# Kernel tuning notes

Measured on AMD Instinct MI355X. Metric: run time of the kernel, lower is better.

## Reference

```python
import jax, jax.numpy as jnp
import numpy as np

DIM = 1024
HEADS = 16
DIM_HEAD = 64
INNER = HEADS * DIM_HEAD
SCALE = DIM_HEAD ** -0.5


def rotate_half(t):
    # '... (j d) -> ... j d' with j=2: split last dim in half
    x1, x2 = jnp.split(t, 2, axis=-1)
    return jnp.concatenate((-x2, x1), axis=-1)


def rotary_pos(n, d, dtype):
    inv_freq = 1.0 / (10000.0 ** (jnp.arange(0, d, 2, dtype=jnp.float32) / d))
    freqs = jnp.arange(n, dtype=jnp.float32)[:, None] * inv_freq[None, :]  # (n, d/2)
    return jnp.concatenate((freqs, freqs), axis=-1).astype(dtype)  # (n, d)


def apply_rope(pos, t):
    return t * jnp.cos(pos) + rotate_half(t) * jnp.sin(pos)


def setup_inputs() -> dict:
    key = jax.random.key(0)
    ks = jax.random.split(key, 5)
    x = jax.random.normal(ks[0], (2, 2048, DIM), dtype=jnp.float32)
    gamma = jnp.ones((DIM,), dtype=jnp.float32)
    beta = jnp.zeros((DIM,), dtype=jnp.float32)
    Wq = jax.random.normal(ks[1], (DIM, INNER), dtype=jnp.float32) * 0.02
    Wkv = jax.random.normal(ks[2], (DIM, 2 * INNER), dtype=jnp.float32) * 0.02
    Wo = jax.random.normal(ks[3], (INNER, DIM), dtype=jnp.float32) * 0.02
    return {"x": x, "gamma": gamma, "beta": beta, "Wq": Wq, "Wkv": Wkv, "Wo": Wo}


def reference(x, gamma, beta, Wq, Wkv, Wo):
    b, n, _ = x.shape
    # LayerNorm with learned gamma, fixed-zero beta buffer
    mu = jnp.mean(x, axis=-1, keepdims=True)
    var = jnp.var(x, axis=-1, keepdims=True)
    xn = (x - mu) / jnp.sqrt(var + 1e-5) * gamma + beta

    q = xn @ Wq                       # (b, n, inner)
    kv = xn @ Wkv
    k, v = jnp.split(kv, 2, axis=-1)

    def to_heads(t):
        return t.reshape(b, n, HEADS, DIM_HEAD).transpose(0, 2, 1, 3)  # b h n d

    q, k, v = map(to_heads, (q, k, v))

    pos = rotary_pos(n, DIM_HEAD, x.dtype)  # (n, d)
    q = apply_rope(pos, q)
    k = apply_rope(pos, k)

    q = q * SCALE
    sim = jnp.einsum('bhid,bhjd->bhij', q, k)

    neg = -jnp.finfo(sim.dtype).max
    causal_mask = jnp.triu(jnp.ones((n, n), dtype=bool), k=1)
    sim = jnp.where(causal_mask, neg, sim)

    attn = jax.nn.softmax(sim, axis=-1)
    out = jnp.einsum('bhij,bhjd->bhid', attn, v)
    out = out.transpose(0, 2, 1, 3).reshape(b, n, INNER)
    return out @ Wo
```

## Files before the change

kernel.cpp:

```cpp
#include <hip/hip_runtime.h>
#include <stdint.h>

typedef unsigned short u16;
typedef __attribute__((ext_vector_type(8))) short short8;
typedef __attribute__((ext_vector_type(4))) float floatx4;
typedef __attribute__((ext_vector_type(4))) unsigned short u16x4;
typedef __attribute__((ext_vector_type(2))) unsigned int uint2v;

__device__ __forceinline__ float bf2f(u16 v) {
  union { uint32_t u; float f; } x; x.u = ((uint32_t)v) << 16; return x.f;
}
__device__ __forceinline__ u16 f2bf(float f) {
  union { float f; uint32_t u; } x; x.f = f;
  uint32_t r = x.u + 0x7fffu + ((x.u >> 16) & 1u);
  return (u16)(r >> 16);
}
__device__ __forceinline__ uint32_t fu(float f) {
  union { float f; uint32_t u; } x; x.f = f; return x.u;
}

#define GL2LDS(g, l)                                                          \
  __builtin_amdgcn_global_load_lds(                                           \
      (const __attribute__((address_space(1))) void*)(g),                     \
      (__attribute__((address_space(3))) void*)(l), 16, 0, 0)

__global__ __launch_bounds__(256) void transpose_w3_k(const float* __restrict__ Wq,
                                                      const float* __restrict__ Wkv,
                                                      const float* __restrict__ Wo,
                                                      u16* __restrict__ wqkvT,
                                                      u16* __restrict__ woT) {
  __shared__ float tile[32][33];
  int z = blockIdx.z;
  const float* in = (z == 0) ? Wq : (z == 1) ? Wkv : Wo;
  u16* out = (z == 0) ? wqkvT : (z == 1) ? (wqkvT + 1024 * 1024) : woT;
  int C = (z == 1) ? 2048 : 1024;
  int c0 = blockIdx.x * 32, r0 = blockIdx.y * 32;
  if (c0 >= C) return;
  int tx = threadIdx.x, ty = threadIdx.y;
#pragma unroll
  for (int i = 0; i < 32; i += 8)
    tile[ty + i][tx] = in[(size_t)(r0 + ty + i) * C + c0 + tx];
  __syncthreads();
#pragma unroll
  for (int i = 0; i < 32; i += 8)
    out[(size_t)(c0 + ty + i) * 1024 + r0 + tx] = f2bf(tile[tx][ty + i]);
}

__global__ __launch_bounds__(256) void layernorm_k(const float* __restrict__ x,
                                                   const float* __restrict__ gamma,
                                                   const float* __restrict__ beta,
                                                   u16* __restrict__ xn) {
  int row = blockIdx.x;
  int t = threadIdx.x;
  const float* xr = x + (size_t)row * 1024;
  float4 xv = *(const float4*)(xr + t * 4);
  float v0 = xv.x, v1 = xv.y, v2 = xv.z, v3 = xv.w;
  float s = v0 + v1 + v2 + v3;
  float s2 = v0 * v0 + v1 * v1 + v2 * v2 + v3 * v3;
#pragma unroll
  for (int d = 1; d < 64; d <<= 1) {
    s += __shfl_xor(s, d, 64);
    s2 += __shfl_xor(s2, d, 64);
  }
  __shared__ float red[8];
  int lane = t & 63, wv = t >> 6;
  if (lane == 0) { red[wv] = s; red[4 + wv] = s2; }
  __syncthreads();
  s = red[0] + red[1] + red[2] + red[3];
  s2 = red[4] + red[5] + red[6] + red[7];
  float mu = s * (1.0f / 1024.0f);
  float var = s2 * (1.0f / 1024.0f) - mu * mu;
  float rstd = rsqrtf(var + 1e-5f);
  float4 gv = *(const float4*)(gamma + t * 4);
  float4 bv = *(const float4*)(beta + t * 4);
  u16x4 ov;
  ov.x = f2bf((v0 - mu) * rstd * gv.x + bv.x);
  ov.y = f2bf((v1 - mu) * rstd * gv.y + bv.y);
  ov.z = f2bf((v2 - mu) * rstd * gv.z + bv.z);
  ov.w = f2bf((v3 - mu) * rstd * gv.w + bv.w);
  *(u16x4*)(xn + (size_t)row * 1024 + t * 4) = ov;
}

__global__ __launch_bounds__(256) void gemm_bf16_k(const u16* __restrict__ A,
                                                   const u16* __restrict__ BT,
                                                   void* __restrict__ Cp,
                                                   int K, int lda, int ldc,
                                                   int f32out) {
  __shared__ __align__(16) u16 lA[128 * 32];
  __shared__ __align__(16) u16 lB[128 * 32];
  int tid = threadIdx.x;
  int bm = blockIdx.y * 128;
  int bn = blockIdx.x * 128;
  int w = tid >> 6, l = tid & 63;
  int wm = (w >> 1) * 64, wn = (w & 1) * 64;
  int lr = l & 15, lq = l >> 4;
  floatx4 acc[4][4] = {};
  int sr = w * 16 + (l >> 2);
  int sc = (l & 3) * 8;
  for (int k0 = 0; k0 < K; k0 += 32) {
    GL2LDS(A + (size_t)(bm + sr) * lda + k0 + sc, &lA[sr * 32 + sc]);
    GL2LDS(A + (size_t)(bm + sr + 64) * lda + k0 + sc, &lA[(sr + 64) * 32 + sc]);
    GL2LDS(BT + (size_t)(bn + sr) * K + k0 + sc, &lB[sr * 32 + sc]);
    GL2LDS(BT + (size_t)(bn + sr + 64) * K + k0 + sc, &lB[(sr + 64) * 32 + sc]);
    __syncthreads();
    short8 afr[4], bfr[4];
#pragma unroll
    for (int i = 0; i < 4; i++)
      afr[i] = *(const short8*)(&lA[(wm + i * 16 + lr) * 32 + lq * 8]);
#pragma unroll
    for (int i = 0; i < 4; i++)
      bfr[i] = *(const short8*)(&lB[(wn + i * 16 + lr) * 32 + lq * 8]);
#pragma unroll
    for (int mi = 0; mi < 4; mi++)
#pragma unroll
      for (int ni = 0; ni < 4; ni++)
        acc[mi][ni] = __builtin_amdgcn_mfma_f32_16x16x32_bf16(
            afr[mi], bfr[ni], acc[mi][ni], 0, 0, 0);
    __syncthreads();
  }
  if (f32out) {
    float* Cf = (float*)Cp;
#pragma unroll
    for (int mi = 0; mi < 4; mi++)
#pragma unroll
      for (int ni = 0; ni < 4; ni++)
#pragma unroll
        for (int r = 0; r < 4; r++) {
          int row = bm + wm + mi * 16 + lq * 4 + r;
          int col = bn + wn + ni * 16 + lr;
          Cf[(size_t)row * ldc + col] = acc[mi][ni][r];
        }
  } else {
    u16* Cb = (u16*)Cp;
#pragma unroll
    for (int mi = 0; mi < 4; mi++)
#pragma unroll
      for (int ni = 0; ni < 4; ni++)
#pragma unroll
        for (int r = 0; r < 4; r++) {
          int row = bm + wm + mi * 16 + lq * 4 + r;
          int col = bn + wn + ni * 16 + lr;
          Cb[(size_t)row * ldc + col] = f2bf(acc[mi][ni][r]);
        }
  }
}

__global__ __launch_bounds__(256) void gemm64_bf16_k(const u16* __restrict__ A,
                                                     const u16* __restrict__ BT,
                                                     float* __restrict__ C,
                                                     int K, int lda, int ldc) {
  __shared__ __align__(16) u16 lA[64 * 32];
  __shared__ __align__(16) u16 lB[128 * 32];
  int tid = threadIdx.x;
  int bm = blockIdx.y * 64;
  int bn = blockIdx.x * 128;
  int w = tid >> 6, l = tid & 63;
  int wm = (w >> 1) * 32, wn = (w & 1) * 64;
  int lr = l & 15, lq = l >> 4;
  floatx4 acc[2][4] = {};
  int sr = w * 16 + (l >> 2);
  int sc = (l & 3) * 8;
  for (int k0 = 0; k0 < K; k0 += 32) {
    GL2LDS(A + (size_t)(bm + sr) * lda + k0 + sc, &lA[sr * 32 + sc]);
    GL2LDS(BT + (size_t)(bn + sr) * K + k0 + sc, &lB[sr * 32 + sc]);
    GL2LDS(BT + (size_t)(bn + sr + 64) * K + k0 + sc, &lB[(sr + 64) * 32 + sc]);
    __syncthreads();
    short8 afr[2], bfr[4];
#pragma unroll
    for (int i = 0; i < 2; i++)
      afr[i] = *(const short8*)(&lA[(wm + i * 16 + lr) * 32 + lq * 8]);
#pragma unroll
    for (int i = 0; i < 4; i++)
      bfr[i] = *(const short8*)(&lB[(wn + i * 16 + lr) * 32 + lq * 8]);
#pragma unroll
    for (int mi = 0; mi < 2; mi++)
#pragma unroll
      for (int ni = 0; ni < 4; ni++)
        acc[mi][ni] = __builtin_amdgcn_mfma_f32_16x16x32_bf16(
            afr[mi], bfr[ni], acc[mi][ni], 0, 0, 0);
    __syncthreads();
  }
#pragma unroll
  for (int mi = 0; mi < 2; mi++)
#pragma unroll
    for (int ni = 0; ni < 4; ni++)
#pragma unroll
      for (int r = 0; r < 4; r++) {
        int row = bm + wm + mi * 16 + lq * 4 + r;
        int col = bn + wn + ni * 16 + lr;
        C[(size_t)row * ldc + col] = acc[mi][ni][r];
      }
}

__global__ __launch_bounds__(256) void rope_vt_k(u16* __restrict__ qkv,
                                                 u16* __restrict__ vT) {
  int bid = blockIdx.x;
  if (bid < 2048) {
    int idx = bid * 256 + threadIdx.x;
    int ig = idx & 7;
    int h = (idx >> 3) & 15;
    int row = idx >> 7;
    int n = row & 2047;
    int i0 = ig * 4;
    const float QS = 0.125f * 1.44269504088896f;
    float c_[4], s_[4];
    float invf = exp2f(-(float)i0 * 0.4152410118609203f);
    const float rstep = 0.74989420933245582f;
#pragma unroll
    for (int e = 0; e < 4; e++) {
      float ang = (float)n * invf;
      c_[e] = cosf(ang);
      s_[e] = sinf(ang);
      invf *= rstep;
    }
    size_t base = (size_t)row * 3072 + h * 64 + i0;
    u16x4 qlo = *(u16x4*)(qkv + base);
    u16x4 qhi = *(u16x4*)(qkv + base + 32);
    u16x4 klo = *(u16x4*)(qkv + base + 1024);
    u16x4 khi = *(u16x4*)(qkv + base + 1056);
    u16x4 oqlo, oqhi, oklo, okhi;
#pragma unroll
    for (int e = 0; e < 4; e++) {
      float x1 = bf2f(((u16*)&qlo)[e]), x2 = bf2f(((u16*)&qhi)[e]);
      ((u16*)&oqlo)[e] = f2bf((x1 * c_[e] - x2 * s_[e]) * QS);
      ((u16*)&oqhi)[e] = f2bf((x2 * c_[e] + x1 * s_[e]) * QS);
      x1 = bf2f(((u16*)&klo)[e]); x2 = bf2f(((u16*)&khi)[e]);
      ((u16*)&oklo)[e] = f2bf(x1 * c_[e] - x2 * s_[e]);
      ((u16*)&okhi)[e] = f2bf(x2 * c_[e] + x1 * s_[e]);
    }
    *(u16x4*)(qkv + base) = oqlo;
    *(u16x4*)(qkv + base + 32) = oqhi;
    *(u16x4*)(qkv + base + 1024) = oklo;
    *(u16x4*)(qkv + base + 1056) = okhi;
  } else {
    __shared__ u16 tile[32][33];
    int vb = bid - 2048;
    int bh = vb >> 7;
    int rest = vb & 127;
    int d0 = (rest >> 6) * 32;
    int n0 = (rest & 63) * 32;
    int b = bh >> 4, h = bh & 15;
    int tid = threadIdx.x;
    int tx = tid & 31, ty = tid >> 5;
#pragma unroll
    for (int i = 0; i < 32; i += 8)
      tile[ty + i][tx] =
          qkv[(size_t)(b * 2048 + n0 + ty + i) * 3072 + 2048 + h * 64 + d0 + tx];
    __syncthreads();
#pragma unroll
    for (int i = 0; i < 32; i += 8)
      vT[((size_t)bh * 64 + d0 + ty + i) * 2048 + n0 + tx] = tile[tx][ty + i];
  }
}

#define LPT 72
__device__ __forceinline__ void attn_tile2(const short8 kf[4][2],
                                           const short8 vf[4][2], u16* lp,
                                           const short8* aq, floatx4* o,
                                           float& m_i, float& l_i, int lr, int lq,
                                           bool diag, int q0, int k0g,
                                           short8 ones) {
  floatx4 s[4];
#pragma unroll
  for (int ni = 0; ni < 4; ni++) {
    floatx4 a = {};
#pragma unroll
    for (int kc = 0; kc < 2; kc++)
      a = __builtin_amdgcn_mfma_f32_16x16x32_bf16(kf[ni][kc], aq[kc], a, 0, 0, 0);
    s[ni] = a;
  }
  if (diag) {
    int qg = q0 + lr;
#pragma unroll
    for (int ni = 0; ni < 4; ni++)
#pragma unroll
      for (int r = 0; r < 4; r++) {
        int kg = k0g + ni * 16 + lq * 4 + r;
        if (kg > qg) s[ni][r] = -1e30f;
      }
  }
  float mx = fmaxf(fmaxf(s[0][0], s[0][1]), fmaxf(s[0][2], s[0][3]));
#pragma unroll
  for (int ni = 1; ni < 4; ni++)
    mx = fmaxf(mx, fmaxf(fmaxf(s[ni][0], s[ni][1]), fmaxf(s[ni][2], s[ni][3])));
  mx = fmaxf(mx, __shfl_xor(mx, 16, 64));
  mx = fmaxf(mx, __shfl_xor(mx, 32, 64));
  float mnew = fmaxf(m_i, mx);
  float alpha = exp2f(m_i - mnew);
  m_i = mnew;
#pragma unroll
  for (int ni = 0; ni < 4; ni++) {
    float p0 = exp2f(s[ni][0] - mnew), p1 = exp2f(s[ni][1] - mnew);
    float p2 = exp2f(s[ni][2] - mnew), p3 = exp2f(s[ni][3] - mnew);
    uint2v dw;
    dw.x = __builtin_amdgcn_perm(fu(p1), fu(p0), 0x07060302u);
    dw.y = __builtin_amdgcn_perm(fu(p3), fu(p2), 0x07060302u);
    *(uint2v*)&lp[lr * LPT + ni * 16 + lq * 4] = dw;
  }
  short8 pb0 = *(const short8*)&lp[lr * LPT + lq * 8];
  short8 pb1 = *(const short8*)&lp[lr * LPT + 32 + lq * 8];
  floatx4 z = {};
  z = __builtin_amdgcn_mfma_f32_16x16x32_bf16(ones, pb0, z, 0, 0, 0);
  z = __builtin_amdgcn_mfma_f32_16x16x32_bf16(ones, pb1, z, 0, 0, 0);
  l_i = l_i * alpha + z[0];
#pragma unroll
  for (int di = 0; di < 4; di++)
#pragma unroll
    for (int r = 0; r < 4; r++) o[di][r] *= alpha;
#pragma unroll
  for (int di = 0; di < 4; di++) {
    o[di] = __builtin_amdgcn_mfma_f32_16x16x32_bf16(vf[di][0], pb0, o[di], 0, 0, 0);
    o[di] = __builtin_amdgcn_mfma_f32_16x16x32_bf16(vf[di][1], pb1, o[di], 0, 0, 0);
  }
}

__global__ __launch_bounds__(256) void attn_k(const u16* __restrict__ qkv,
                                              const u16* __restrict__ vt,
                                              u16* __restrict__ out) {
  __shared__ __align__(16) u16 lK[2][64 * 64];
  __shared__ __align__(16) u16 lV[2][64 * 64];
  __shared__ __align__(16) u16 lPA[4][16 * LPT];
  __shared__ __align__(16) u16 lPB[4][16 * LPT];
  int bh = blockIdx.y;
  int b = bh >> 4, h = bh & 15;
  int p = blockIdx.x;
  int jB = 31 - p;
  int tid = threadIdx.x;
  int w = tid >> 6, l = tid & 63;
  int lr = l & 15, lq = l >> 4;
  int q0A = p * 64 + w * 16;
  int q0B = jB * 64 + w * 16;
  const u16* qb = qkv + (size_t)b * 2048 * 3072 + h * 64;
  const u16* kb = qkv + (size_t)b * 2048 * 3072 + 1024 + h * 64;
  const u16* vb = vt + (size_t)bh * 64 * 2048;
  short8 aqA[2], aqB[2];
  aqA[0] = *(const short8*)(qb + (size_t)(q0A + lr) * 3072 + lq * 8);
  aqA[1] = *(const short8*)(qb + (size_t)(q0A + lr) * 3072 + 32 + lq * 8);
  aqB[0] = *(const short8*)(qb + (size_t)(q0B + lr) * 3072 + lq * 8);
  aqB[1] = *(const short8*)(qb + (size_t)(q0B + lr) * 3072 + 32 + lq * 8);
  short8 ones;
#pragma unroll
  for (int i = 0; i < 8; i++) ones[i] = (short)0x3F80;
  floatx4 oA[4] = {}, oB[4] = {};
  float mA = -1e30f, lA_ = 0.0f, mB = -1e30f, lB_ = 0.0f;
  int srow8 = l >> 3;
  int sc8 = (l & 7) ^ srow8;
  auto stage = [&](int bufi, int kt) {
#pragma unroll
    for (int c = 0; c < 2; c++) {
      int m = w + c * 4;
      int row = m * 8 + srow8;
      GL2LDS(kb + (size_t)(kt * 64 + row) * 3072 + sc8 * 8, &lK[bufi][m * 512]);
      GL2LDS(vb + (size_t)row * 2048 + kt * 64 + sc8 * 8, &lV[bufi][m * 512]);
    }
  };
  stage(0, 0);
  for (int kt = 0; kt <= jB; ++kt) {
    int cur = kt & 1;
    __syncthreads();
    if (kt < jB) stage(cur ^ 1, kt + 1);
    short8 kf[4][2], vf[4][2];
#pragma unroll
    for (int ni = 0; ni < 4; ni++) {
      int R = ni * 16 + lr;
      int c80 = (lq ^ (R & 7)) * 8;
      int c81 = ((4 + lq) ^ (R & 7)) * 8;
      kf[ni][0] = *(const short8*)&lK[cur][R * 64 + c80];
      kf[ni][1] = *(const short8*)&lK[cur][R * 64 + c81];
      vf[ni][0] = *(const short8*)&lV[cur][R * 64 + c80];
      vf[ni][1] = *(const short8*)&lV[cur][R * 64 + c81];
    }
    attn_tile2(kf, vf, &lPB[w][0], aqB, oB, mB, lB_, lr, lq, kt == jB, q0B,
               kt * 64, ones);
    if (kt <= p)
      attn_tile2(kf, vf, &lPA[w][0], aqA, oA, mA, lA_, lr, lq, kt == p, q0A,
                 kt * 64, ones);
  }
  float rlA = 1.0f / lA_, rlB = 1.0f / lB_;
#pragma unroll
  for (int di = 0; di < 4; di++) {
    uint2v dwA, dwB;
    u16 a0 = f2bf(oA[di][0] * rlA), a1 = f2bf(oA[di][1] * rlA);
    u16 a2 = f2bf(oA[di][2] * rlA), a3 = f2bf(oA[di][3] * rlA);
    dwA.x = (uint32_t)a0 | ((uint32_t)a1 << 16);
    dwA.y = (uint32_t)a2 | ((uint32_t)a3 << 16);
    u16 b0 = f2bf(oB[di][0] * rlB), b1 = f2bf(oB[di][1] * rlB);
    u16 b2 = f2bf(oB[di][2] * rlB), b3 = f2bf(oB[di][3] * rlB);
    dwB.x = (uint32_t)b0 | ((uint32_t)b1 << 16);
    dwB.y = (uint32_t)b2 | ((uint32_t)b3 << 16);
    int dcol = h * 64 + di * 16 + lq * 4;
    *(uint2v*)(out + ((size_t)(b * 2048 + q0A + lr)) * 3072 + dcol) = dwA;
    *(uint2v*)(out + ((size_t)(b * 2048 + q0B + lr)) * 3072 + dcol) = dwB;
  }
}

extern "C" void kernel_launch(void* const* d_in, const int* in_sizes, int n_in,
                              void* d_out, int out_size, void* d_ws, size_t ws_size,
                              hipStream_t stream) {
  const float* x = (const float*)d_in[0];
  const float* gamma = (const float*)d_in[1];
  const float* beta = (const float*)d_in[2];
  const float* Wq = (const float*)d_in[3];
  const float* Wkv = (const float*)d_in[4];
  const float* Wo = (const float*)d_in[5];
  float* out = (float*)d_out;
  char* ws = (char*)d_ws;

  u16* qkv = (u16*)(ws);
  u16* wqkvT = (u16*)(ws + 25165824);
  u16* woT = (u16*)(ws + 31457280);
  u16* xn = (u16*)(ws + 33554432);
  u16* vT = xn;
  u16* attn_out = qkv + 2048;

  dim3 tb32(32, 8);
  transpose_w3_k<<<dim3(64, 32, 3), tb32, 0, stream>>>(Wq, Wkv, Wo, wqkvT, woT);
  layernorm_k<<<4096, 256, 0, stream>>>(x, gamma, beta, xn);
  gemm_bf16_k<<<dim3(24, 32), 256, 0, stream>>>(xn, wqkvT, qkv, 1024, 1024, 3072, 0);
  rope_vt_k<<<6144, 256, 0, stream>>>(qkv, vT);
  attn_k<<<dim3(16, 32), 256, 0, stream>>>(qkv, vT, attn_out);
  gemm64_bf16_k<<<dim3(8, 64), 256, 0, stream>>>(attn_out, woT, out, 1024, 3072, 1024);
}
```

Before: 215.9 us.

## Split paired causal q-tiles into one tile per block, single-buffered K/V

Replaces the paired-query-tile scheme (each block handled tile p and 31-p to balance causal work) with one 64-row query tile per block over a doubled grid, using a rotated tile index to spread work across blocks. K/V staging becomes single-buffered with two barriers per iteration instead of double-buffered prefetch. K and V fragments are read from LDS just before use. This raises block count and cuts LDS and registers for higher occupancy, but gives up load overlap and K/V reuse across two query tiles, and leaves blocks with uneven causal work.

```diff
diff --git a/kernel.cpp b/kernel.cpp
--- a/kernel.cpp
+++ b/kernel.cpp
@@ -254,143 +254,115 @@
 }
 
 #define LPT 72
-__device__ __forceinline__ void attn_tile2(const short8 kf[4][2],
-                                           const short8 vf[4][2], u16* lp,
-                                           const short8* aq, floatx4* o,
-                                           float& m_i, float& l_i, int lr, int lq,
-                                           bool diag, int q0, int k0g,
-                                           short8 ones) {
-  floatx4 s[4];
-#pragma unroll
-  for (int ni = 0; ni < 4; ni++) {
-    floatx4 a = {};
-#pragma unroll
-    for (int kc = 0; kc < 2; kc++)
-      a = __builtin_amdgcn_mfma_f32_16x16x32_bf16(kf[ni][kc], aq[kc], a, 0, 0, 0);
-    s[ni] = a;
-  }
-  if (diag) {
-    int qg = q0 + lr;
-#pragma unroll
-    for (int ni = 0; ni < 4; ni++)
-#pragma unroll
-      for (int r = 0; r < 4; r++) {
-        int kg = k0g + ni * 16 + lq * 4 + r;
-        if (kg > qg) s[ni][r] = -1e30f;
-      }
-  }
-  float mx = fmaxf(fmaxf(s[0][0], s[0][1]), fmaxf(s[0][2], s[0][3]));
-#pragma unroll
-  for (int ni = 1; ni < 4; ni++)
-    mx = fmaxf(mx, fmaxf(fmaxf(s[ni][0], s[ni][1]), fmaxf(s[ni][2], s[ni][3])));
-  mx = fmaxf(mx, __shfl_xor(mx, 16, 64));
-  mx = fmaxf(mx, __shfl_xor(mx, 32, 64));
-  float mnew = fmaxf(m_i, mx);
-  float alpha = exp2f(m_i - mnew);
-  m_i = mnew;
-#pragma unroll
-  for (int ni = 0; ni < 4; ni++) {
-    float p0 = exp2f(s[ni][0] - mnew), p1 = exp2f(s[ni][1] - mnew);
-    float p2 = exp2f(s[ni][2] - mnew), p3 = exp2f(s[ni][3] - mnew);
-    uint2v dw;
-    dw.x = __builtin_amdgcn_perm(fu(p1), fu(p0), 0x07060302u);
-    dw.y = __builtin_amdgcn_perm(fu(p3), fu(p2), 0x07060302u);
-    *(uint2v*)&lp[lr * LPT + ni * 16 + lq * 4] = dw;
-  }
-  short8 pb0 = *(const short8*)&lp[lr * LPT + lq * 8];
-  short8 pb1 = *(const short8*)&lp[lr * LPT + 32 + lq * 8];
-  floatx4 z = {};
-  z = __builtin_amdgcn_mfma_f32_16x16x32_bf16(ones, pb0, z, 0, 0, 0);
-  z = __builtin_amdgcn_mfma_f32_16x16x32_bf16(ones, pb1, z, 0, 0, 0);
-  l_i = l_i * alpha + z[0];
-#pragma unroll
-  for (int di = 0; di < 4; di++)
-#pragma unroll
-    for (int r = 0; r < 4; r++) o[di][r] *= alpha;
-#pragma unroll
-  for (int di = 0; di < 4; di++) {
-    o[di] = __builtin_amdgcn_mfma_f32_16x16x32_bf16(vf[di][0], pb0, o[di], 0, 0, 0);
-    o[di] = __builtin_amdgcn_mfma_f32_16x16x32_bf16(vf[di][1], pb1, o[di], 0, 0, 0);
-  }
-}
-
 __global__ __launch_bounds__(256) void attn_k(const u16* __restrict__ qkv,
                                               const u16* __restrict__ vt,
                                               u16* __restrict__ out) {
-  __shared__ __align__(16) u16 lK[2][64 * 64];
-  __shared__ __align__(16) u16 lV[2][64 * 64];
-  __shared__ __align__(16) u16 lPA[4][16 * LPT];
-  __shared__ __align__(16) u16 lPB[4][16 * LPT];
+  __shared__ __align__(16) u16 lK[64 * 64];
+  __shared__ __align__(16) u16 lV[64 * 64];
+  __shared__ __align__(16) u16 lP[4][16 * LPT];
   int bh = blockIdx.y;
   int b = bh >> 4, h = bh & 15;
-  int p = blockIdx.x;
-  int jB = 31 - p;
+  int qt = (blockIdx.x + bh) & 31;
   int tid = threadIdx.x;
   int w = tid >> 6, l = tid & 63;
   int lr = l & 15, lq = l >> 4;
-  int q0A = p * 64 + w * 16;
-  int q0B = jB * 64 + w * 16;
+  int q0 = qt * 64 + w * 16;
   const u16* qb = qkv + (size_t)b * 2048 * 3072 + h * 64;
   const u16* kb = qkv + (size_t)b * 2048 * 3072 + 1024 + h * 64;
   const u16* vb = vt + (size_t)bh * 64 * 2048;
-  short8 aqA[2], aqB[2];
-  aqA[0] = *(const short8*)(qb + (size_t)(q0A + lr) * 3072 + lq * 8);
-  aqA[1] = *(const short8*)(qb + (size_t)(q0A + lr) * 3072 + 32 + lq * 8);
-  aqB[0] = *(const short8*)(qb + (size_t)(q0B + lr) * 3072 + lq * 8);
-  aqB[1] = *(const short8*)(qb + (size_t)(q0B + lr) * 3072 + 32 + lq * 8);
+  short8 aq[2];
+  aq[0] = *(const short8*)(qb + (size_t)(q0 + lr) * 3072 + lq * 8);
+  aq[1] = *(const short8*)(qb + (size_t)(q0 + lr) * 3072 + 32 + lq * 8);
   short8 ones;
 #pragma unroll
   for (int i = 0; i < 8; i++) ones[i] = (short)0x3F80;
-  floatx4 oA[4] = {}, oB[4] = {};
-  float mA = -1e30f, lA_ = 0.0f, mB = -1e30f, lB_ = 0.0f;
+  floatx4 o[4] = {};
+  float m_i = -1e30f, l_i = 0.0f;
   int srow8 = l >> 3;
   int sc8 = (l & 7) ^ srow8;
-  auto stage = [&](int bufi, int kt) {
+  u16* lp = &lP[w][0];
+  for (int kt = 0; kt <= qt; ++kt) {
 #pragma unroll
     for (int c = 0; c < 2; c++) {
       int m = w + c * 4;
       int row = m * 8 + srow8;
-      GL2LDS(kb + (size_t)(kt * 64 + row) * 3072 + sc8 * 8, &lK[bufi][m * 512]);
-      GL2LDS(vb + (size_t)row * 2048 + kt * 64 + sc8 * 8, &lV[bufi][m * 512]);
-    }
-  };
-  stage(0, 0);
-  for (int kt = 0; kt <= jB; ++kt) {
-    int cur = kt & 1;
-    __syncthreads();
-    if (kt < jB) stage(cur ^ 1, kt + 1);
-    short8 kf[4][2], vf[4][2];
+      GL2LDS(kb + (size_t)(kt * 64 + row) * 3072 + sc8 * 8, &lK[m * 512]);
+      GL2LDS(vb + (size_t)row * 2048 + kt * 64 + sc8 * 8, &lV[m * 512]);
+    }
+    __syncthreads();
+    floatx4 s[4];
 #pragma unroll
     for (int ni = 0; ni < 4; ni++) {
-      int R = ni * 16 + lr;
+      floatx4 a = {};
+#pragma unroll
+      for (int kc = 0; kc < 2; kc++) {
+        int R = ni * 16 + lr;
+        int c8 = (kc * 4 + lq) ^ (R & 7);
+        short8 kf = *(const short8*)&lK[R * 64 + c8 * 8];
+        a = __builtin_amdgcn_mfma_f32_16x16x32_bf16(kf, aq[kc], a, 0, 0, 0);
+      }
+      s[ni] = a;
+    }
+    if (kt == qt) {
+      int qg = q0 + lr;
+#pragma unroll
+      for (int ni = 0; ni < 4; ni++)
+#pragma unroll
+        for (int r = 0; r < 4; r++) {
+          int kg = kt * 64 + ni * 16 + lq * 4 + r;
+          if (kg > qg) s[ni][r] = -1e30f;
+        }
+    }
+    float mx = fmaxf(fmaxf(s[0][0], s[0][1]), fmaxf(s[0][2], s[0][3]));
+#pragma unroll
+    for (int ni = 1; ni < 4; ni++)
+      mx = fmaxf(mx, fmaxf(fmaxf(s[ni][0], s[ni][1]), fmaxf(s[ni][2], s[ni][3])));
+    mx = fmaxf(mx, __shfl_xor(mx, 16, 64));
+    mx = fmaxf(mx, __shfl_xor(mx, 32, 64));
+    float mnew = fmaxf(m_i, mx);
+    float alpha = exp2f(m_i - mnew);
+    m_i = mnew;
+#pragma unroll
+    for (int ni = 0; ni < 4; ni++) {
+      float p0 = exp2f(s[ni][0] - mnew), p1 = exp2f(s[ni][1] - mnew);
+      float p2 = exp2f(s[ni][2] - mnew), p3 = exp2f(s[ni][3] - mnew);
+      uint2v dw;
+      dw.x = __builtin_amdgcn_perm(fu(p1), fu(p0), 0x07060302u);
+      dw.y = __builtin_amdgcn_perm(fu(p3), fu(p2), 0x07060302u);
+      *(uint2v*)&lp[lr * LPT + ni * 16 + lq * 4] = dw;
+    }
+    short8 pb0 = *(const short8*)&lp[lr * LPT + lq * 8];
+    short8 pb1 = *(const short8*)&lp[lr * LPT + 32 + lq * 8];
+    floatx4 z = {};
+    z = __builtin_amdgcn_mfma_f32_16x16x32_bf16(ones, pb0, z, 0, 0, 0);
+    z = __builtin_amdgcn_mfma_f32_16x16x32_bf16(ones, pb1, z, 0, 0, 0);
+    l_i = l_i * alpha + z[0];
+#pragma unroll
+    for (int di = 0; di < 4; di++)
+#pragma unroll
+      for (int r = 0; r < 4; r++) o[di][r] *= alpha;
+#pragma unroll
+    for (int di = 0; di < 4; di++) {
+      int R = di * 16 + lr;
       int c80 = (lq ^ (R & 7)) * 8;
       int c81 = ((4 + lq) ^ (R & 7)) * 8;
-      kf[ni][0] = *(const short8*)&lK[cur][R * 64 + c80];
-      kf[ni][1] = *(const short8*)&lK[cur][R * 64 + c81];
-      vf[ni][0] = *(const short8*)&lV[cur][R * 64 + c80];
-      vf[ni][1] = *(const short8*)&lV[cur][R * 64 + c81];
-    }
-    attn_tile2(kf, vf, &lPB[w][0], aqB, oB, mB, lB_, lr, lq, kt == jB, q0B,
-               kt * 64, ones);
-    if (kt <= p)
-      attn_tile2(kf, vf, &lPA[w][0], aqA, oA, mA, lA_, lr, lq, kt == p, q0A,
-                 kt * 64, ones);
-  }
-  float rlA = 1.0f / lA_, rlB = 1.0f / lB_;
+      short8 v0 = *(const short8*)&lV[R * 64 + c80];
+      o[di] = __builtin_amdgcn_mfma_f32_16x16x32_bf16(v0, pb0, o[di], 0, 0, 0);
+      short8 v1 = *(const short8*)&lV[R * 64 + c81];
+      o[di] = __builtin_amdgcn_mfma_f32_16x16x32_bf16(v1, pb1, o[di], 0, 0, 0);
+    }
+    __syncthreads();
+  }
+  float rl = 1.0f / l_i;
 #pragma unroll
   for (int di = 0; di < 4; di++) {
-    uint2v dwA, dwB;
-    u16 a0 = f2bf(oA[di][0] * rlA), a1 = f2bf(oA[di][1] * rlA);
-    u16 a2 = f2bf(oA[di][2] * rlA), a3 = f2bf(oA[di][3] * rlA);
-    dwA.x = (uint32_t)a0 | ((uint32_t)a1 << 16);
-    dwA.y = (uint32_t)a2 | ((uint32_t)a3 << 16);
-    u16 b0 = f2bf(oB[di][0] * rlB), b1 = f2bf(oB[di][1] * rlB);
-    u16 b2 = f2bf(oB[di][2] * rlB), b3 = f2bf(oB[di][3] * rlB);
-    dwB.x = (uint32_t)b0 | ((uint32_t)b1 << 16);
-    dwB.y = (uint32_t)b2 | ((uint32_t)b3 << 16);
+    uint2v dw;
+    u16 a0 = f2bf(o[di][0] * rl), a1 = f2bf(o[di][1] * rl);
+    u16 a2 = f2bf(o[di][2] * rl), a3 = f2bf(o[di][3] * rl);
+    dw.x = (uint32_t)a0 | ((uint32_t)a1 << 16);
+    dw.y = (uint32_t)a2 | ((uint32_t)a3 << 16);
     int dcol = h * 64 + di * 16 + lq * 4;
-    *(uint2v*)(out + ((size_t)(b * 2048 + q0A + lr)) * 3072 + dcol) = dwA;
-    *(uint2v*)(out + ((size_t)(b * 2048 + q0B + lr)) * 3072 + dcol) = dwB;
+    *(uint2v*)(out + ((size_t)(b * 2048 + q0 + lr)) * 3072 + dcol) = dw;
   }
 }
 
@@ -418,6 +390,6 @@
   layernorm_k<<<4096, 256, 0, stream>>>(x, gamma, beta, xn);
   gemm_bf16_k<<<dim3(24, 32), 256, 0, stream>>>(xn, wqkvT, qkv, 1024, 1024, 3072, 0);
   rope_vt_k<<<6144, 256, 0, stream>>>(qkv, vT);
-  attn_k<<<dim3(16, 32), 256, 0, stream>>>(qkv, vT, attn_out);
+  attn_k<<<dim3(32, 32), 256, 0, stream>>>(qkv, vT, attn_out);
   gemm64_bf16_k<<<dim3(8, 64), 256, 0, stream>>>(attn_out, woT, out, 1024, 3072, 1024);
 }
```

After: 227.4 us. +5.3%, slower.
